# Performance work log

Measured on AMD Instinct MI355X. Metric: run time of the kernel, lower is better.

The kernel has to match this reference:

```python
import jax, jax.numpy as jnp
import numpy as np

N, F_IN, E = 50000, 128, 800000
HID, HEADS, EMB = 32, 8, 64
NEG_SLOPE = 0.2


def gat_conv(x, src, dst, W_src, W_dst, att_src, att_dst, bias, heads, out_ch, concat):
    n = x.shape[0]
    h_src = (x @ W_src).reshape(n, heads, out_ch)   # [N,H,C]
    h_dst = (x @ W_dst).reshape(n, heads, out_ch)
    a_src = jnp.sum(h_src * att_src, axis=-1)       # [N,H]
    a_dst = jnp.sum(h_dst * att_dst, axis=-1)
    e = jax.nn.leaky_relu(a_src[src] + a_dst[dst], NEG_SLOPE)  # [E,H]
    # segment softmax over destination nodes (stable, max detached as in PyG)
    m = jax.ops.segment_max(e, dst, num_segments=n)
    m = jnp.where(jnp.isfinite(m), m, 0.0)
    ex = jnp.exp(e - jax.lax.stop_gradient(m)[dst])
    denom = jax.ops.segment_sum(ex, dst, num_segments=n)
    alpha = ex / (denom[dst] + 1e-16)               # [E,H]
    msg = h_src[src] * alpha[:, :, None]            # [E,H,C]
    out = jax.ops.segment_sum(msg, dst, num_segments=n)  # [N,H,C]
    if concat:
        out = out.reshape(n, heads * out_ch)
    else:
        out = out.mean(axis=1)
    return out + bias


def setup_inputs() -> dict:
    key = jax.random.key(0)
    ks = jax.random.split(key, 12)
    g = lambda k, shape: jax.random.normal(k, shape, dtype=jnp.float32) * (1.0 / np.sqrt(shape[0]))
    x = jax.random.normal(ks[0], (N, F_IN), dtype=jnp.float32)
    edge_index = jax.random.randint(ks[1], (2, E), 0, N, dtype=jnp.int64)
    return {
        "x": x,
        "edge_index": edge_index,
        "W_src1": g(ks[2], (F_IN, HEADS * HID)),
        "W_dst1": g(ks[3], (F_IN, HEADS * HID)),
        "att_src1": g(ks[4], (HEADS, HID)) * 0.1,
        "att_dst1": g(ks[5], (HEADS, HID)) * 0.1,
        "b1": jnp.zeros((HEADS * HID,), dtype=jnp.float32),
        "W_src2": g(ks[6], (HEADS * HID, EMB)),
        "W_dst2": g(ks[7], (HEADS * HID, EMB)),
        "att_src2": g(ks[8], (1, EMB)) * 0.1,
        "att_dst2": g(ks[9], (1, EMB)) * 0.1,
        "b2": jnp.zeros((EMB,), dtype=jnp.float32),
    }


def reference(x, edge_index, W_src1, W_dst1, att_src1, att_dst1, b1,
              W_src2, W_dst2, att_src2, att_dst2, b2):
    src, dst = edge_index[0], edge_index[1]
    h = gat_conv(x, src, dst, W_src1, W_dst1, att_src1, att_dst1, b1, HEADS, HID, True)
    h = jax.nn.relu(h)
    out = gat_conv(h, src, dst, W_src2, W_dst2, att_src2, att_dst2, b2, 1, EMB, False)
    return out
```

## Files before the change

### kernel.cpp

```cpp
#include <hip/hip_runtime.h>
#include <hip/hip_bf16.h>
#include <cstdint>
#include <cstddef>

#define NN    50000
#define FIN   128
#define EE    800000
#define HID_  32
#define HEADS_ 8
#define EMB_  64
#define NEG   0.2f
#define NB_SCAN 196
#define NB_PREP 202
#define NB_EDGE 3125
#define NB_GEMM1 1564
#define LOG2E 1.4426950408889634f

typedef short bf16x8 __attribute__((ext_vector_type(8)));
typedef float f32x4  __attribute__((ext_vector_type(4)));

static __device__ __forceinline__ ushort f2bf(float f){
    uint u = __float_as_uint(f);
    uint r = (u + 0x7FFFu + ((u >> 16) & 1u)) >> 16;
    return (ushort)r;
}
static __device__ __forceinline__ float bf2f(ushort u){
    return __uint_as_float(((uint)u) << 16);
}
static __device__ __forceinline__ float pexp(float t){
    return __builtin_amdgcn_exp2f(fmaxf(t, NEG * t));
}

__global__ __launch_bounds__(256) void k_prep_hist(const float* __restrict__ Wsrc1, const float* __restrict__ Wdst1,
                                                   const float* __restrict__ asrc1, const float* __restrict__ adst1,
                                                   const float* __restrict__ Wsrc2, const float* __restrict__ Wdst2,
                                                   const float* __restrict__ asrc2, const float* __restrict__ adst2,
                                                   ushort* __restrict__ wt1bf, float* __restrict__ wt2,
                                                   ushort* __restrict__ w1t, ushort* __restrict__ w2t,
                                                   const int* __restrict__ dst, int* __restrict__ deg,
                                                   int* __restrict__ rank){
    if (blockIdx.x >= NB_PREP){
        int e = (blockIdx.x - NB_PREP) * 256 + threadIdx.x;
        if (e < EE) rank[e] = atomicAdd(&deg[dst[e]], 1);
        return;
    }
    int idx = blockIdx.x * blockDim.x + threadIdx.x;
    if (idx < 2048){
        int f = idx >> 4, j = idx & 15;
        const float* W; const float* a; int h;
        if (j < 8) { W = Wsrc1; a = asrc1; h = j; } else { W = Wdst1; a = adst1; h = j - 8; }
        float s = 0.f;
        #pragma unroll
        for (int c = 0; c < HID_; ++c)
            s += W[(size_t)f * (HEADS_ * HID_) + h * HID_ + c] * a[h * HID_ + c];
        wt1bf[j * 128 + f] = f2bf(s * LOG2E);
    } else if (idx < 2560){
        int t = idx - 2048;
        int f = t >> 1, j = t & 1;
        const float* W = j ? Wdst2 : Wsrc2;
        const float* a = j ? adst2 : asrc2;
        float s = 0.f;
        #pragma unroll
        for (int c = 0; c < EMB_; ++c) s += W[(size_t)f * EMB_ + c] * a[c];
        wt2[j * 256 + f] = s * LOG2E;
    } else if (idx < 35328){
        int t = idx - 2560;
        int n = t >> 7, k = t & 127;
        w1t[t] = f2bf(Wsrc1[(size_t)k * 256 + n]);
    } else if (idx < 51712){
        int t = idx - 35328;
        int n = t >> 8, k = t & 255;
        w2t[t] = f2bf(Wsrc2[(size_t)k * 64 + n]);
    }
}

__global__ __launch_bounds__(256) void k_scanall(const int* __restrict__ deg, int* __restrict__ row_ptr,
                                                 int* __restrict__ bsum, int* __restrict__ flags){
    __shared__ int s[256];
    __shared__ int ps[256];
    int tid = threadIdx.x, b = blockIdx.x;
    int i = b * 256 + tid;
    int v = (i < NN) ? deg[i] : 0;
    s[tid] = v;
    __syncthreads();
    #pragma unroll
    for (int off = 1; off < 256; off <<= 1){
        int t = (tid >= off) ? s[tid - off] : 0;
        __syncthreads();
        s[tid] += t;
        __syncthreads();
    }
    if (tid == 255){
        bsum[b] = s[255];
        __hip_atomic_store(&flags[b], 1, __ATOMIC_RELEASE, __HIP_MEMORY_SCOPE_AGENT);
    }
    int p = 0;
    if (tid < b){
        while (__hip_atomic_load(&flags[tid], __ATOMIC_ACQUIRE, __HIP_MEMORY_SCOPE_AGENT) == 0){}
        p = bsum[tid];
    }
    ps[tid] = p;
    __syncthreads();
    #pragma unroll
    for (int off = 128; off > 0; off >>= 1){
        if (tid < off) ps[tid] += ps[tid + off];
        __syncthreads();
    }
    int boff = ps[0];
    if (i < NN) row_ptr[i] = boff + s[tid] - v;
    if (b == 0 && tid == 0) row_ptr[NN] = EE;
}

__global__ __launch_bounds__(256) void k_gemm1_scatter(const float* __restrict__ x,
                                                       const ushort* __restrict__ w1t,
                                                       const ushort* __restrict__ wt1bf,
                                                       ushort* __restrict__ c,
                                                       float* __restrict__ a_src1,
                                                       float* __restrict__ a_dst1,
                                                       const int* __restrict__ src, const int* __restrict__ dstp,
                                                       const int* __restrict__ row_ptr, const int* __restrict__ rank,
                                                       int* __restrict__ col){
    __shared__ ushort As[64][136];
    __shared__ ushort Bs[128][136];
    __shared__ ushort Bsa[16][136];
    if (blockIdx.x >= NB_GEMM1){
        int e = (blockIdx.x - NB_GEMM1) * 256 + threadIdx.x;
        if (e < EE){
            int d = dstp[e];
            col[row_ptr[d] + rank[e]] = src[e];
        }
        return;
    }
    const int tid = threadIdx.x;
    const int m0 = (blockIdx.x >> 1) * 64;
    const int n0 = (blockIdx.x & 1) * 128;
    #pragma unroll
    for (int i = 0; i < 8; ++i){
        int idx = tid + i * 256;
        int r = idx >> 5, c4 = idx & 31;
        int m = m0 + r;
        float4 v = make_float4(0.f, 0.f, 0.f, 0.f);
        if (m < NN) v = *(const float4*)&x[(size_t)m * FIN + c4 * 4];
        ushort4 u; u.x = f2bf(v.x); u.y = f2bf(v.y); u.z = f2bf(v.z); u.w = f2bf(v.w);
        *(ushort4*)&As[r][c4 * 4] = u;
    }
    #pragma unroll
    for (int i = 0; i < 8; ++i){
        int idx = tid + i * 256;
        int r = idx >> 4, c8 = idx & 15;
        const ushort4* s4 = (const ushort4*)&w1t[(size_t)(n0 + r) * 128 + c8 * 8];
        *(ushort4*)&Bs[r][c8 * 8]     = s4[0];
        *(ushort4*)&Bs[r][c8 * 8 + 4] = s4[1];
    }
    if (n0 == 0){
        int r = tid >> 4, c8 = tid & 15;
        const ushort4* s4 = (const ushort4*)&wt1bf[r * 128 + c8 * 8];
        *(ushort4*)&Bsa[r][c8 * 8]     = s4[0];
        *(ushort4*)&Bsa[r][c8 * 8 + 4] = s4[1];
    }
    __syncthreads();
    const int lane = tid & 63;
    const int w    = tid >> 6;
    const int mr   = lane & 15;
    const int kg   = lane >> 4;
    f32x4 acc[8];
    #pragma unroll
    for (int i = 0; i < 8; ++i) acc[i] = (f32x4){0.f, 0.f, 0.f, 0.f};
    f32x4 acca = (f32x4){0.f, 0.f, 0.f, 0.f};
    #pragma unroll
    for (int ks = 0; ks < 4; ++ks){
        bf16x8 a = *(const bf16x8*)&As[w * 16 + mr][ks * 32 + kg * 8];
        #pragma unroll
        for (int nf = 0; nf < 8; ++nf){
            bf16x8 b = *(const bf16x8*)&Bs[nf * 16 + mr][ks * 32 + kg * 8];
            acc[nf] = __builtin_amdgcn_mfma_f32_16x16x32_bf16(a, b, acc[nf], 0, 0, 0);
        }
        if (n0 == 0){
            bf16x8 ba = *(const bf16x8*)&Bsa[mr][ks * 32 + kg * 8];
            acca = __builtin_amdgcn_mfma_f32_16x16x32_bf16(a, ba, acca, 0, 0, 0);
        }
    }
    #pragma unroll
    for (int nf = 0; nf < 8; ++nf){
        int colb = n0 + nf * 16 + mr;
        #pragma unroll
        for (int r = 0; r < 4; ++r){
            int row = m0 + w * 16 + kg * 4 + r;
            if (row < NN) c[(size_t)row * 256 + colb] = f2bf(acc[nf][r]);
        }
    }
    if (n0 == 0){
        int j = mr;
        #pragma unroll
        for (int r = 0; r < 4; ++r){
            int row = m0 + w * 16 + kg * 4 + r;
            if (row < NN){
                if (j < 8) a_src1[(size_t)row * 8 + j]       = acca[r];
                else       a_dst1[(size_t)row * 8 + (j - 8)] = acca[r];
            }
        }
    }
}

__global__ __launch_bounds__(256) void k_gemm2_mfma(const ushort* __restrict__ hbf,
                                                    const ushort* __restrict__ w2t,
                                                    ushort* __restrict__ c2){
    __shared__ ushort As[64][264];
    __shared__ ushort Bs[64][264];
    const int tid = threadIdx.x;
    const int m0 = blockIdx.x * 64;
    #pragma unroll
    for (int i = 0; i < 8; ++i){
        int idx = tid + i * 256;
        int r = idx >> 5, c8 = idx & 31;
        int m = m0 + r;
        ushort4 v0 = make_ushort4(0,0,0,0), v1 = make_ushort4(0,0,0,0);
        if (m < NN){
            const ushort4* s4 = (const ushort4*)&hbf[(size_t)m * 256 + c8 * 8];
            v0 = s4[0]; v1 = s4[1];
        }
        *(ushort4*)&As[r][c8 * 8]     = v0;
        *(ushort4*)&As[r][c8 * 8 + 4] = v1;
    }
    #pragma unroll
    for (int i = 0; i < 8; ++i){
        int idx = tid + i * 256;
        int r = idx >> 5, c8 = idx & 31;
        const ushort4* s4 = (const ushort4*)&w2t[(size_t)r * 256 + c8 * 8];
        *(ushort4*)&Bs[r][c8 * 8]     = s4[0];
        *(ushort4*)&Bs[r][c8 * 8 + 4] = s4[1];
    }
    __syncthreads();
    const int lane = tid & 63;
    const int w    = tid >> 6;
    const int mr   = lane & 15;
    const int kg   = lane >> 4;
    f32x4 acc[4];
    #pragma unroll
    for (int i = 0; i < 4; ++i) acc[i] = (f32x4){0.f, 0.f, 0.f, 0.f};
    #pragma unroll
    for (int ks = 0; ks < 8; ++ks){
        bf16x8 a = *(const bf16x8*)&As[w * 16 + mr][ks * 32 + kg * 8];
        #pragma unroll
        for (int nf = 0; nf < 4; ++nf){
            bf16x8 b = *(const bf16x8*)&Bs[nf * 16 + mr][ks * 32 + kg * 8];
            acc[nf] = __builtin_amdgcn_mfma_f32_16x16x32_bf16(a, b, acc[nf], 0, 0, 0);
        }
    }
    #pragma unroll
    for (int nf = 0; nf < 4; ++nf){
        int colb = nf * 16 + mr;
        #pragma unroll
        for (int r = 0; r < 4; ++r){
            int row = m0 + w * 16 + kg * 4 + r;
            if (row < NN) c2[(size_t)row * 64 + colb] = f2bf(acc[nf][r]);
        }
    }
}

__global__ __launch_bounds__(256) void k_agg1(const ushort* __restrict__ hsrc, const float* __restrict__ a_src,
                                              const float* __restrict__ a_dst, const int* __restrict__ row_ptr,
                                              const int* __restrict__ col, const float* __restrict__ b1,
                                              const float* __restrict__ wt2,
                                              ushort* __restrict__ hout_bf,
                                              float* __restrict__ a_src2, float* __restrict__ a_dst2){
    int node = blockIdx.x * 4 + (threadIdx.x >> 6);
    if (node >= NN) return;
    int lane = threadIdx.x & 63;
    int head = lane >> 3;
    float ad = a_dst[(size_t)node * 8 + head];
    const ushort4* h4 = (const ushort4*)hsrc;
    float4 acc = make_float4(0.f, 0.f, 0.f, 0.f);
    float den = 0.f;
    int b = row_ptr[node], en = row_ptr[node + 1];
    int i = b;
    for (; i + 4 <= en; i += 4){
        int s0 = col[i], s1 = col[i+1], s2 = col[i+2], s3 = col[i+3];
        float e0 = a_src[(size_t)s0 * 8 + head];
        float e1 = a_src[(size_t)s1 * 8 + head];
        float e2 = a_src[(size_t)s2 * 8 + head];
        float e3 = a_src[(size_t)s3 * 8 + head];
        ushort4 v0 = h4[(size_t)s0 * 64 + lane];
        ushort4 v1 = h4[(size_t)s1 * 64 + lane];
        ushort4 v2 = h4[(size_t)s2 * 64 + lane];
        ushort4 v3 = h4[(size_t)s3 * 64 + lane];
        float p0 = pexp(e0 + ad);
        float p1 = pexp(e1 + ad);
        float p2 = pexp(e2 + ad);
        float p3 = pexp(e3 + ad);
        acc.x += p0*bf2f(v0.x) + p1*bf2f(v1.x) + p2*bf2f(v2.x) + p3*bf2f(v3.x);
        acc.y += p0*bf2f(v0.y) + p1*bf2f(v1.y) + p2*bf2f(v2.y) + p3*bf2f(v3.y);
        acc.z += p0*bf2f(v0.z) + p1*bf2f(v1.z) + p2*bf2f(v2.z) + p3*bf2f(v3.z);
        acc.w += p0*bf2f(v0.w) + p1*bf2f(v1.w) + p2*bf2f(v2.w) + p3*bf2f(v3.w);
        den += p0 + p1 + p2 + p3;
    }
    for (; i < en; ++i){
        int s = col[i];
        float p = pexp(a_src[(size_t)s * 8 + head] + ad);
        ushort4 v = h4[(size_t)s * 64 + lane];
        acc.x += p * bf2f(v.x); acc.y += p * bf2f(v.y);
        acc.z += p * bf2f(v.z); acc.w += p * bf2f(v.w);
        den += p;
    }
    float inv = 1.f / (den + 1e-16f);
    float4 bb = ((const float4*)b1)[lane];
    float4 o;
    o.x = fmaxf(acc.x * inv + bb.x, 0.f);
    o.y = fmaxf(acc.y * inv + bb.y, 0.f);
    o.z = fmaxf(acc.z * inv + bb.z, 0.f);
    o.w = fmaxf(acc.w * inv + bb.w, 0.f);
    ushort4 ob; ob.x = f2bf(o.x); ob.y = f2bf(o.y); ob.z = f2bf(o.z); ob.w = f2bf(o.w);
    ((ushort4*)hout_bf)[(size_t)node * 64 + lane] = ob;
    float4 ws4 = ((const float4*)wt2)[lane];
    float4 wd4 = ((const float4*)(wt2 + 256))[lane];
    float ss2 = o.x*ws4.x + o.y*ws4.y + o.z*ws4.z + o.w*ws4.w;
    float sd2 = o.x*wd4.x + o.y*wd4.y + o.z*wd4.z + o.w*wd4.w;
    #pragma unroll
    for (int off = 32; off > 0; off >>= 1){
        ss2 += __shfl_xor(ss2, off);
        sd2 += __shfl_xor(sd2, off);
    }
    if (lane == 0){ a_src2[node] = ss2; a_dst2[node] = sd2; }
}

__global__ __launch_bounds__(256) void k_agg2(const ushort* __restrict__ h2bf, const float* __restrict__ a_src2,
                                              const float* __restrict__ a_dst2, const int* __restrict__ row_ptr,
                                              const int* __restrict__ col, const float* __restrict__ b2,
                                              float* __restrict__ out){
    int node = blockIdx.x * 4 + (threadIdx.x >> 6);
    if (node >= NN) return;
    int lane = threadIdx.x & 63;
    float ad = a_dst2[node];
    float acc = 0.f, den = 0.f;
    int b = row_ptr[node], en = row_ptr[node + 1];
    int i = b;
    for (; i + 4 <= en; i += 4){
        int s0 = col[i], s1 = col[i+1], s2 = col[i+2], s3 = col[i+3];
        float e0 = a_src2[s0], e1 = a_src2[s1], e2 = a_src2[s2], e3 = a_src2[s3];
        ushort u0 = h2bf[(size_t)s0 * 64 + lane];
        ushort u1 = h2bf[(size_t)s1 * 64 + lane];
        ushort u2 = h2bf[(size_t)s2 * 64 + lane];
        ushort u3 = h2bf[(size_t)s3 * 64 + lane];
        float p0 = pexp(e0 + ad);
        float p1 = pexp(e1 + ad);
        float p2 = pexp(e2 + ad);
        float p3 = pexp(e3 + ad);
        acc += p0*bf2f(u0) + p1*bf2f(u1) + p2*bf2f(u2) + p3*bf2f(u3);
        den += p0 + p1 + p2 + p3;
    }
    for (; i < en; ++i){
        int s = col[i];
        float p = pexp(a_src2[s] + ad);
        acc += p * bf2f(h2bf[(size_t)s * 64 + lane]);
        den += p;
    }
    out[(size_t)node * 64 + lane] = acc / (den + 1e-16f) + b2[lane];
}

extern "C" void kernel_launch(void* const* d_in, const int* in_sizes, int n_in,
                              void* d_out, int out_size, void* d_ws, size_t ws_size,
                              hipStream_t stream){
    const float* x        = (const float*)d_in[0];
    const int*   ei       = (const int*)  d_in[1];
    const float* Wsrc1    = (const float*)d_in[2];
    const float* Wdst1    = (const float*)d_in[3];
    const float* att_src1 = (const float*)d_in[4];
    const float* att_dst1 = (const float*)d_in[5];
    const float* b1       = (const float*)d_in[6];
    const float* Wsrc2    = (const float*)d_in[7];
    const float* Wdst2    = (const float*)d_in[8];
    const float* att_src2 = (const float*)d_in[9];
    const float* att_dst2 = (const float*)d_in[10];
    const float* b2       = (const float*)d_in[11];
    float* out = (float*)d_out;
    const int* srcp = ei;
    const int* dstp = ei + EE;

    char* base = (char*)d_ws;
    ushort* hbf1   = (ushort*)base;  base += (size_t)NN * 256 * 2;
    ushort* hrel   = (ushort*)base;  base += (size_t)NN * 256 * 2;
    ushort* h2bf   = (ushort*)base;  base += (size_t)NN * 64 * 2;
    float*  a_src1 = (float*)base;   base += (size_t)NN * 8 * 4;
    float*  a_dst1 = (float*)base;   base += (size_t)NN * 8 * 4;
    float*  a_src2 = (float*)base;   base += (size_t)NN * 4;
    float*  a_dst2 = (float*)base;   base += (size_t)NN * 4;
    ushort* wt1bf  = (ushort*)base;  base += 2048 * 2;
    float*  wt2    = (float*)base;   base += 512 * 4;
    ushort* w1t    = (ushort*)base;  base += 32768 * 2;
    ushort* w2t    = (ushort*)base;  base += 16384 * 2;
    int* deg     = (int*)base;       base += (size_t)NN * 4;
    int* flags   = (int*)base;       base += 256 * 4;
    int* row_ptr = (int*)base;       base += (size_t)(NN + 1) * 4;
    int* rank    = (int*)base;       base += (size_t)EE * 4;
    int* col     = (int*)base;       base += (size_t)EE * 4;
    int* bsum    = (int*)base;       base += 256 * 4;

    (void)hipMemsetAsync(deg, 0, (NN + 256) * sizeof(int), stream);

    k_prep_hist<<<NB_PREP + NB_EDGE, 256, 0, stream>>>(Wsrc1, Wdst1, att_src1, att_dst1,
                                                       Wsrc2, Wdst2, att_src2, att_dst2,
                                                       wt1bf, wt2, w1t, w2t,
                                                       dstp, deg, rank);
    k_scanall<<<NB_SCAN, 256, 0, stream>>>(deg, row_ptr, bsum, flags);
    k_gemm1_scatter<<<NB_GEMM1 + NB_EDGE, 256, 0, stream>>>(x, w1t, wt1bf, hbf1, a_src1, a_dst1,
                                                            srcp, dstp, row_ptr, rank, col);
    k_agg1<<<(NN + 3) / 4, 256, 0, stream>>>(hbf1, a_src1, a_dst1, row_ptr, col, b1, wt2,
                                             hrel, a_src2, a_dst2);
    k_gemm2_mfma<<<(NN + 63) / 64, 256, 0, stream>>>(hrel, w2t, h2bf);
    k_agg2<<<(NN + 3) / 4, 256, 0, stream>>>(h2bf, a_src2, a_dst2, row_ptr, col, b2, out);
}
```

Before: 202.7 us.

## Fuse layer-2 GEMM into agg1, overlap GEMM1 half with scan, use cursor scatter

```diff
diff --git a/kernel.cpp b/kernel.cpp
--- a/kernel.cpp
+++ b/kernel.cpp
@@ -13,7 +13,7 @@
 #define NB_SCAN 196
 #define NB_PREP 202
 #define NB_EDGE 3125
-#define NB_GEMM1 1564
+#define NB_M1   782
 #define LOG2E 1.4426950408889634f
 
 typedef short bf16x8 __attribute__((ext_vector_type(8)));
@@ -37,11 +37,10 @@
                                                    const float* __restrict__ asrc2, const float* __restrict__ adst2,
                                                    ushort* __restrict__ wt1bf, float* __restrict__ wt2,
                                                    ushort* __restrict__ w1t, ushort* __restrict__ w2t,
-                                                   const int* __restrict__ dst, int* __restrict__ deg,
-                                                   int* __restrict__ rank){
+                                                   const int* __restrict__ dst, int* __restrict__ deg){
     if (blockIdx.x >= NB_PREP){
         int e = (blockIdx.x - NB_PREP) * 256 + threadIdx.x;
-        if (e < EE) rank[e] = atomicAdd(&deg[dst[e]], 1);
+        if (e < EE) atomicAdd(&deg[dst[e]], 1);
         return;
     }
     int idx = blockIdx.x * blockDim.x + threadIdx.x;
@@ -74,66 +73,51 @@
     }
 }
 
-__global__ __launch_bounds__(256) void k_scanall(const int* __restrict__ deg, int* __restrict__ row_ptr,
-                                                 int* __restrict__ bsum, int* __restrict__ flags){
+__global__ __launch_bounds__(256) void k_scan_gemm1b(const int* __restrict__ deg, int* __restrict__ row_ptr,
+                                                     int* __restrict__ cursor, int* __restrict__ bsum,
+                                                     int* __restrict__ flags,
+                                                     const float* __restrict__ x, const ushort* __restrict__ w1t,
+                                                     ushort* __restrict__ c){
     __shared__ int s[256];
     __shared__ int ps[256];
-    int tid = threadIdx.x, b = blockIdx.x;
-    int i = b * 256 + tid;
-    int v = (i < NN) ? deg[i] : 0;
-    s[tid] = v;
-    __syncthreads();
-    #pragma unroll
-    for (int off = 1; off < 256; off <<= 1){
-        int t = (tid >= off) ? s[tid - off] : 0;
-        __syncthreads();
-        s[tid] += t;
-        __syncthreads();
-    }
-    if (tid == 255){
-        bsum[b] = s[255];
-        __hip_atomic_store(&flags[b], 1, __ATOMIC_RELEASE, __HIP_MEMORY_SCOPE_AGENT);
-    }
-    int p = 0;
-    if (tid < b){
-        while (__hip_atomic_load(&flags[tid], __ATOMIC_ACQUIRE, __HIP_MEMORY_SCOPE_AGENT) == 0){}
-        p = bsum[tid];
-    }
-    ps[tid] = p;
-    __syncthreads();
-    #pragma unroll
-    for (int off = 128; off > 0; off >>= 1){
-        if (tid < off) ps[tid] += ps[tid + off];
-        __syncthreads();
-    }
-    int boff = ps[0];
-    if (i < NN) row_ptr[i] = boff + s[tid] - v;
-    if (b == 0 && tid == 0) row_ptr[NN] = EE;
-}
-
-__global__ __launch_bounds__(256) void k_gemm1_scatter(const float* __restrict__ x,
-                                                       const ushort* __restrict__ w1t,
-                                                       const ushort* __restrict__ wt1bf,
-                                                       ushort* __restrict__ c,
-                                                       float* __restrict__ a_src1,
-                                                       float* __restrict__ a_dst1,
-                                                       const int* __restrict__ src, const int* __restrict__ dstp,
-                                                       const int* __restrict__ row_ptr, const int* __restrict__ rank,
-                                                       int* __restrict__ col){
     __shared__ ushort As[64][136];
     __shared__ ushort Bs[128][136];
-    __shared__ ushort Bsa[16][136];
-    if (blockIdx.x >= NB_GEMM1){
-        int e = (blockIdx.x - NB_GEMM1) * 256 + threadIdx.x;
-        if (e < EE){
-            int d = dstp[e];
-            col[row_ptr[d] + rank[e]] = src[e];
-        }
+    const int tid = threadIdx.x;
+    if (blockIdx.x < NB_SCAN){
+        int b = blockIdx.x;
+        int i = b * 256 + tid;
+        int v = (i < NN) ? deg[i] : 0;
+        s[tid] = v;
+        __syncthreads();
+        #pragma unroll
+        for (int off = 1; off < 256; off <<= 1){
+            int t = (tid >= off) ? s[tid - off] : 0;
+            __syncthreads();
+            s[tid] += t;
+            __syncthreads();
+        }
+        if (tid == 255){
+            bsum[b] = s[255];
+            __hip_atomic_store(&flags[b], 1, __ATOMIC_RELEASE, __HIP_MEMORY_SCOPE_AGENT);
+        }
+        int p = 0;
+        if (tid < b){
+            while (__hip_atomic_load(&flags[tid], __ATOMIC_ACQUIRE, __HIP_MEMORY_SCOPE_AGENT) == 0){}
+            p = bsum[tid];
+        }
+        ps[tid] = p;
+        __syncthreads();
+        #pragma unroll
+        for (int off = 128; off > 0; off >>= 1){
+            if (tid < off) ps[tid] += ps[tid + off];
+            __syncthreads();
+        }
+        int val = ps[0] + s[tid] - v;
+        if (i < NN){ row_ptr[i] = val; cursor[i] = val; }
+        if (b == 0 && tid == 0) row_ptr[NN] = EE;
         return;
     }
-    const int tid = threadIdx.x;
-    const int m0 = (blockIdx.x >> 1) * 64;
-    const int n0 = (blockIdx.x & 1) * 128;
+    const int m0 = (blockIdx.x - NB_SCAN) * 64;
     #pragma unroll
     for (int i = 0; i < 8; ++i){
         int idx = tid + i * 256;
@@ -148,15 +132,9 @@
     for (int i = 0; i < 8; ++i){
         int idx = tid + i * 256;
         int r = idx >> 4, c8 = idx & 15;
-        const ushort4* s4 = (const ushort4*)&w1t[(size_t)(n0 + r) * 128 + c8 * 8];
+        const ushort4* s4 = (const ushort4*)&w1t[(size_t)(128 + r) * 128 + c8 * 8];
         *(ushort4*)&Bs[r][c8 * 8]     = s4[0];
         *(ushort4*)&Bs[r][c8 * 8 + 4] = s4[1];
-    }
-    if (n0 == 0){
-        int r = tid >> 4, c8 = tid & 15;
-        const ushort4* s4 = (const ushort4*)&wt1bf[r * 128 + c8 * 8];
-        *(ushort4*)&Bsa[r][c8 * 8]     = s4[0];
-        *(ushort4*)&Bsa[r][c8 * 8 + 4] = s4[1];
     }
     __syncthreads();
     const int lane = tid & 63;
@@ -166,7 +144,6 @@
     f32x4 acc[8];
     #pragma unroll
     for (int i = 0; i < 8; ++i) acc[i] = (f32x4){0.f, 0.f, 0.f, 0.f};
-    f32x4 acca = (f32x4){0.f, 0.f, 0.f, 0.f};
     #pragma unroll
     for (int ks = 0; ks < 4; ++ks){
         bf16x8 a = *(const bf16x8*)&As[w * 16 + mr][ks * 32 + kg * 8];
@@ -175,21 +152,94 @@
             bf16x8 b = *(const bf16x8*)&Bs[nf * 16 + mr][ks * 32 + kg * 8];
             acc[nf] = __builtin_amdgcn_mfma_f32_16x16x32_bf16(a, b, acc[nf], 0, 0, 0);
         }
-        if (n0 == 0){
-            bf16x8 ba = *(const bf16x8*)&Bsa[mr][ks * 32 + kg * 8];
-            acca = __builtin_amdgcn_mfma_f32_16x16x32_bf16(a, ba, acca, 0, 0, 0);
-        }
     }
     #pragma unroll
     for (int nf = 0; nf < 8; ++nf){
-        int colb = n0 + nf * 16 + mr;
+        int colb = 128 + nf * 16 + mr;
         #pragma unroll
         for (int r = 0; r < 4; ++r){
             int row = m0 + w * 16 + kg * 4 + r;
             if (row < NN) c[(size_t)row * 256 + colb] = f2bf(acc[nf][r]);
         }
     }
-    if (n0 == 0){
+}
+
+__global__ __launch_bounds__(256) void k_gemm1a_scatter(const float* __restrict__ x,
+                                                        const ushort* __restrict__ w1t,
+                                                        const ushort* __restrict__ wt1bf,
+                                                        ushort* __restrict__ c,
+                                                        float* __restrict__ a_src1,
+                                                        float* __restrict__ a_dst1,
+                                                        const int* __restrict__ src, const int* __restrict__ dstp,
+                                                        int* __restrict__ cursor, int* __restrict__ col){
+    __shared__ ushort As[64][136];
+    __shared__ ushort Bs[128][136];
+    __shared__ ushort Bsa[16][136];
+    if (blockIdx.x >= NB_M1){
+        int e = (blockIdx.x - NB_M1) * 256 + threadIdx.x;
+        if (e < EE){
+            int d = dstp[e];
+            int pos = atomicAdd(&cursor[d], 1);
+            col[pos] = src[e];
+        }
+        return;
+    }
+    const int tid = threadIdx.x;
+    const int m0 = blockIdx.x * 64;
+    #pragma unroll
+    for (int i = 0; i < 8; ++i){
+        int idx = tid + i * 256;
+        int r = idx >> 5, c4 = idx & 31;
+        int m = m0 + r;
+        float4 v = make_float4(0.f, 0.f, 0.f, 0.f);
+        if (m < NN) v = *(const float4*)&x[(size_t)m * FIN + c4 * 4];
+        ushort4 u; u.x = f2bf(v.x); u.y = f2bf(v.y); u.z = f2bf(v.z); u.w = f2bf(v.w);
+        *(ushort4*)&As[r][c4 * 4] = u;
+    }
+    #pragma unroll
+    for (int i = 0; i < 8; ++i){
+        int idx = tid + i * 256;
+        int r = idx >> 4, c8 = idx & 15;
+        const ushort4* s4 = (const ushort4*)&w1t[(size_t)r * 128 + c8 * 8];
+        *(ushort4*)&Bs[r][c8 * 8]     = s4[0];
+        *(ushort4*)&Bs[r][c8 * 8 + 4] = s4[1];
+    }
+    {
+        int r = tid >> 4, c8 = tid & 15;
+        const ushort4* s4 = (const ushort4*)&wt1bf[r * 128 + c8 * 8];
+        *(ushort4*)&Bsa[r][c8 * 8]     = s4[0];
+        *(ushort4*)&Bsa[r][c8 * 8 + 4] = s4[1];
+    }
+    __syncthreads();
+    const int lane = tid & 63;
+    const int w    = tid >> 6;
+    const int mr   = lane & 15;
+    const int kg   = lane >> 4;
+    f32x4 acc[8];
+    #pragma unroll
+    for (int i = 0; i < 8; ++i) acc[i] = (f32x4){0.f, 0.f, 0.f, 0.f};
+    f32x4 acca = (f32x4){0.f, 0.f, 0.f, 0.f};
+    #pragma unroll
+    for (int ks = 0; ks < 4; ++ks){
+        bf16x8 a = *(const bf16x8*)&As[w * 16 + mr][ks * 32 + kg * 8];
+        #pragma unroll
+        for (int nf = 0; nf < 8; ++nf){
+            bf16x8 b = *(const bf16x8*)&Bs[nf * 16 + mr][ks * 32 + kg * 8];
+            acc[nf] = __builtin_amdgcn_mfma_f32_16x16x32_bf16(a, b, acc[nf], 0, 0, 0);
+        }
+        bf16x8 ba = *(const bf16x8*)&Bsa[mr][ks * 32 + kg * 8];
+        acca = __builtin_amdgcn_mfma_f32_16x16x32_bf16(a, ba, acca, 0, 0, 0);
+    }
+    #pragma unroll
+    for (int nf = 0; nf < 8; ++nf){
+        int colb = nf * 16 + mr;
+        #pragma unroll
+        for (int r = 0; r < 4; ++r){
+            int row = m0 + w * 16 + kg * 4 + r;
+            if (row < NN) c[(size_t)row * 256 + colb] = f2bf(acc[nf][r]);
+        }
+    }
+    {
         int j = mr;
         #pragma unroll
         for (int r = 0; r < 4; ++r){
@@ -202,72 +252,17 @@
     }
 }
 
-__global__ __launch_bounds__(256) void k_gemm2_mfma(const ushort* __restrict__ hbf,
-                                                    const ushort* __restrict__ w2t,
-                                                    ushort* __restrict__ c2){
-    __shared__ ushort As[64][264];
-    __shared__ ushort Bs[64][264];
-    const int tid = threadIdx.x;
-    const int m0 = blockIdx.x * 64;
-    #pragma unroll
-    for (int i = 0; i < 8; ++i){
-        int idx = tid + i * 256;
-        int r = idx >> 5, c8 = idx & 31;
-        int m = m0 + r;
-        ushort4 v0 = make_ushort4(0,0,0,0), v1 = make_ushort4(0,0,0,0);
-        if (m < NN){
-            const ushort4* s4 = (const ushort4*)&hbf[(size_t)m * 256 + c8 * 8];
-            v0 = s4[0]; v1 = s4[1];
-        }
-        *(ushort4*)&As[r][c8 * 8]     = v0;
-        *(ushort4*)&As[r][c8 * 8 + 4] = v1;
-    }
-    #pragma unroll
-    for (int i = 0; i < 8; ++i){
-        int idx = tid + i * 256;
-        int r = idx >> 5, c8 = idx & 31;
-        const ushort4* s4 = (const ushort4*)&w2t[(size_t)r * 256 + c8 * 8];
-        *(ushort4*)&Bs[r][c8 * 8]     = s4[0];
-        *(ushort4*)&Bs[r][c8 * 8 + 4] = s4[1];
-    }
-    __syncthreads();
-    const int lane = tid & 63;
-    const int w    = tid >> 6;
-    const int mr   = lane & 15;
-    const int kg   = lane >> 4;
-    f32x4 acc[4];
-    #pragma unroll
-    for (int i = 0; i < 4; ++i) acc[i] = (f32x4){0.f, 0.f, 0.f, 0.f};
-    #pragma unroll
-    for (int ks = 0; ks < 8; ++ks){
-        bf16x8 a = *(const bf16x8*)&As[w * 16 + mr][ks * 32 + kg * 8];
-        #pragma unroll
-        for (int nf = 0; nf < 4; ++nf){
-            bf16x8 b = *(const bf16x8*)&Bs[nf * 16 + mr][ks * 32 + kg * 8];
-            acc[nf] = __builtin_amdgcn_mfma_f32_16x16x32_bf16(a, b, acc[nf], 0, 0, 0);
-        }
-    }
-    #pragma unroll
-    for (int nf = 0; nf < 4; ++nf){
-        int colb = nf * 16 + mr;
-        #pragma unroll
-        for (int r = 0; r < 4; ++r){
-            int row = m0 + w * 16 + kg * 4 + r;
-            if (row < NN) c2[(size_t)row * 64 + colb] = f2bf(acc[nf][r]);
-        }
-    }
-}
-
 __global__ __launch_bounds__(256) void k_agg1(const ushort* __restrict__ hsrc, const float* __restrict__ a_src,
                                               const float* __restrict__ a_dst, const int* __restrict__ row_ptr,
                                               const int* __restrict__ col, const float* __restrict__ b1,
-                                              const float* __restrict__ wt2,
-                                              ushort* __restrict__ hout_bf,
+                                              const float* __restrict__ wt2, const ushort* __restrict__ w2t,
+                                              ushort* __restrict__ h2bf,
                                               float* __restrict__ a_src2, float* __restrict__ a_dst2){
-    int node = blockIdx.x * 4 + (threadIdx.x >> 6);
-    if (node >= NN) return;
-    int lane = threadIdx.x & 63;
-    int head = lane >> 3;
+    __shared__ ushort hl[16][264];
+    const int w    = threadIdx.x >> 6;
+    const int node = blockIdx.x * 4 + w;
+    const int lane = threadIdx.x & 63;
+    const int head = lane >> 3;
     float ad = a_dst[(size_t)node * 8 + head];
     const ushort4* h4 = (const ushort4*)hsrc;
     float4 acc = make_float4(0.f, 0.f, 0.f, 0.f);
@@ -309,8 +304,6 @@
     o.y = fmaxf(acc.y * inv + bb.y, 0.f);
     o.z = fmaxf(acc.z * inv + bb.z, 0.f);
     o.w = fmaxf(acc.w * inv + bb.w, 0.f);
-    ushort4 ob; ob.x = f2bf(o.x); ob.y = f2bf(o.y); ob.z = f2bf(o.z); ob.w = f2bf(o.w);
-    ((ushort4*)hout_bf)[(size_t)node * 64 + lane] = ob;
     float4 ws4 = ((const float4*)wt2)[lane];
     float4 wd4 = ((const float4*)(wt2 + 256))[lane];
     float ss2 = o.x*ws4.x + o.y*ws4.y + o.z*ws4.z + o.w*ws4.w;
@@ -321,6 +314,22 @@
         sd2 += __shfl_xor(sd2, off);
     }
     if (lane == 0){ a_src2[node] = ss2; a_dst2[node] = sd2; }
+    ushort4 ob; ob.x = f2bf(o.x); ob.y = f2bf(o.y); ob.z = f2bf(o.z); ob.w = f2bf(o.w);
+    *(ushort4*)&hl[w][lane * 4] = ob;
+    __syncthreads();
+    const int mr = lane & 15, kg = lane >> 4;
+    f32x4 acc2 = (f32x4){0.f, 0.f, 0.f, 0.f};
+    #pragma unroll
+    for (int ks = 0; ks < 8; ++ks){
+        bf16x8 a = *(const bf16x8*)&hl[mr][ks * 32 + kg * 8];
+        bf16x8 bb2 = *(const bf16x8*)&w2t[(size_t)(w * 16 + mr) * 256 + ks * 32 + kg * 8];
+        acc2 = __builtin_amdgcn_mfma_f32_16x16x32_bf16(a, bb2, acc2, 0, 0, 0);
+    }
+    if (kg == 0){
+        #pragma unroll
+        for (int r = 0; r < 4; ++r)
+            h2bf[(size_t)(blockIdx.x * 4 + r) * 64 + w * 16 + mr] = f2bf(acc2[r]);
+    }
 }
 
 __global__ __launch_bounds__(256) void k_agg2(const ushort* __restrict__ h2bf, const float* __restrict__ a_src2,
@@ -334,19 +343,21 @@
     float acc = 0.f, den = 0.f;
     int b = row_ptr[node], en = row_ptr[node + 1];
     int i = b;
-    for (; i + 4 <= en; i += 4){
-        int s0 = col[i], s1 = col[i+1], s2 = col[i+2], s3 = col[i+3];
-        float e0 = a_src2[s0], e1 = a_src2[s1], e2 = a_src2[s2], e3 = a_src2[s3];
-        ushort u0 = h2bf[(size_t)s0 * 64 + lane];
-        ushort u1 = h2bf[(size_t)s1 * 64 + lane];
-        ushort u2 = h2bf[(size_t)s2 * 64 + lane];
-        ushort u3 = h2bf[(size_t)s3 * 64 + lane];
-        float p0 = pexp(e0 + ad);
-        float p1 = pexp(e1 + ad);
-        float p2 = pexp(e2 + ad);
-        float p3 = pexp(e3 + ad);
-        acc += p0*bf2f(u0) + p1*bf2f(u1) + p2*bf2f(u2) + p3*bf2f(u3);
-        den += p0 + p1 + p2 + p3;
+    for (; i + 8 <= en; i += 8){
+        int ss[8]; float e[8]; ushort u[8]; float p[8];
+        #pragma unroll
+        for (int j = 0; j < 8; ++j) ss[j] = col[i + j];
+        #pragma unroll
+        for (int j = 0; j < 8; ++j) e[j] = a_src2[ss[j]];
+        #pragma unroll
+        for (int j = 0; j < 8; ++j) u[j] = h2bf[(size_t)ss[j] * 64 + lane];
+        #pragma unroll
+        for (int j = 0; j < 8; ++j) p[j] = pexp(e[j] + ad);
+        #pragma unroll
+        for (int j = 0; j < 8; ++j){
+            acc += p[j] * bf2f(u[j]);
+            den += p[j];
+        }
     }
     for (; i < en; ++i){
         int s = col[i];
@@ -378,7 +389,6 @@
 
     char* base = (char*)d_ws;
     ushort* hbf1   = (ushort*)base;  base += (size_t)NN * 256 * 2;
-    ushort* hrel   = (ushort*)base;  base += (size_t)NN * 256 * 2;
     ushort* h2bf   = (ushort*)base;  base += (size_t)NN * 64 * 2;
     float*  a_src1 = (float*)base;   base += (size_t)NN * 8 * 4;
     float*  a_dst1 = (float*)base;   base += (size_t)NN * 8 * 4;
@@ -391,7 +401,7 @@
     int* deg     = (int*)base;       base += (size_t)NN * 4;
     int* flags   = (int*)base;       base += 256 * 4;
     int* row_ptr = (int*)base;       base += (size_t)(NN + 1) * 4;
-    int* rank    = (int*)base;       base += (size_t)EE * 4;
+    int* cursor  = (int*)base;       base += (size_t)NN * 4;
     int* col     = (int*)base;       base += (size_t)EE * 4;
     int* bsum    = (int*)base;       base += 256 * 4;
 
@@ -400,12 +410,12 @@
     k_prep_hist<<<NB_PREP + NB_EDGE, 256, 0, stream>>>(Wsrc1, Wdst1, att_src1, att_dst1,
                                                        Wsrc2, Wdst2, att_src2, att_dst2,
                                                        wt1bf, wt2, w1t, w2t,
-                                                       dstp, deg, rank);
-    k_scanall<<<NB_SCAN, 256, 0, stream>>>(deg, row_ptr, bsum, flags);
-    k_gemm1_scatter<<<NB_GEMM1 + NB_EDGE, 256, 0, stream>>>(x, w1t, wt1bf, hbf1, a_src1, a_dst1,
-                                                            srcp, dstp, row_ptr, rank, col);
-    k_agg1<<<(NN + 3) / 4, 256, 0, stream>>>(hbf1, a_src1, a_dst1, row_ptr, col, b1, wt2,
-                                             hrel, a_src2, a_dst2);
-    k_gemm2_mfma<<<(NN + 63) / 64, 256, 0, stream>>>(hrel, w2t, h2bf);
-    k_agg2<<<(NN + 3) / 4, 256, 0, stream>>>(h2bf, a_src2, a_dst2, row_ptr, col, b2, out);
-}
+                                                       dstp, deg);
+    k_scan_gemm1b<<<NB_SCAN + NB_M1, 256, 0, stream>>>(deg, row_ptr, cursor, bsum, flags,
+                                                       x, w1t, hbf1);
+    k_gemm1a_scatter<<<NB_M1 + NB_EDGE, 256, 0, stream>>>(x, w1t, wt1bf, hbf1, a_src1, a_dst1,
+                                                          srcp, dstp, cursor, col);
+    k_agg1<<<NN / 4, 256, 0, stream>>>(hbf1, a_src1, a_dst1, row_ptr, col, b1, wt2, w2t,
+                                       h2bf, a_src2, a_dst2);
+    k_agg2<<<NN / 4, 256, 0, stream>>>(h2bf, a_src2, a_dst2, row_ptr, col, b2, out);
+}
```

New measurement: 265.9 us. 31.2% more time.

## Replace CSR scan and scatter with fixed-capacity per-node edge buckets

Applied to the files above, without the earlier changes.

```diff
diff --git a/kernel.cpp b/kernel.cpp
--- a/kernel.cpp
+++ b/kernel.cpp
@@ -10,10 +10,9 @@
 #define HEADS_ 8
 #define EMB_  64
 #define NEG   0.2f
-#define NB_SCAN 196
+#define CAP   64
 #define NB_PREP 202
 #define NB_EDGE 3125
-#define NB_GEMM1 1564
 #define LOG2E 1.4426950408889634f
 
 typedef short bf16x8 __attribute__((ext_vector_type(8)));
@@ -37,11 +36,15 @@
                                                    const float* __restrict__ asrc2, const float* __restrict__ adst2,
                                                    ushort* __restrict__ wt1bf, float* __restrict__ wt2,
                                                    ushort* __restrict__ w1t, ushort* __restrict__ w2t,
-                                                   const int* __restrict__ dst, int* __restrict__ deg,
-                                                   int* __restrict__ rank){
+                                                   const int* __restrict__ src, const int* __restrict__ dst,
+                                                   int* __restrict__ deg, int* __restrict__ col){
     if (blockIdx.x >= NB_PREP){
         int e = (blockIdx.x - NB_PREP) * 256 + threadIdx.x;
-        if (e < EE) rank[e] = atomicAdd(&deg[dst[e]], 1);
+        if (e < EE){
+            int d = dst[e];
+            int r = atomicAdd(&deg[d], 1);
+            col[d * CAP + r] = src[e];
+        }
         return;
     }
     int idx = blockIdx.x * blockDim.x + threadIdx.x;
@@ -74,66 +77,18 @@
     }
 }
 
-__global__ __launch_bounds__(256) void k_scanall(const int* __restrict__ deg, int* __restrict__ row_ptr,
-                                                 int* __restrict__ bsum, int* __restrict__ flags){
-    __shared__ int s[256];
-    __shared__ int ps[256];
-    int tid = threadIdx.x, b = blockIdx.x;
-    int i = b * 256 + tid;
-    int v = (i < NN) ? deg[i] : 0;
-    s[tid] = v;
-    __syncthreads();
-    #pragma unroll
-    for (int off = 1; off < 256; off <<= 1){
-        int t = (tid >= off) ? s[tid - off] : 0;
-        __syncthreads();
-        s[tid] += t;
-        __syncthreads();
-    }
-    if (tid == 255){
-        bsum[b] = s[255];
-        __hip_atomic_store(&flags[b], 1, __ATOMIC_RELEASE, __HIP_MEMORY_SCOPE_AGENT);
-    }
-    int p = 0;
-    if (tid < b){
-        while (__hip_atomic_load(&flags[tid], __ATOMIC_ACQUIRE, __HIP_MEMORY_SCOPE_AGENT) == 0){}
-        p = bsum[tid];
-    }
-    ps[tid] = p;
-    __syncthreads();
-    #pragma unroll
-    for (int off = 128; off > 0; off >>= 1){
-        if (tid < off) ps[tid] += ps[tid + off];
-        __syncthreads();
-    }
-    int boff = ps[0];
-    if (i < NN) row_ptr[i] = boff + s[tid] - v;
-    if (b == 0 && tid == 0) row_ptr[NN] = EE;
-}
-
-__global__ __launch_bounds__(256) void k_gemm1_scatter(const float* __restrict__ x,
-                                                       const ushort* __restrict__ w1t,
-                                                       const ushort* __restrict__ wt1bf,
-                                                       ushort* __restrict__ c,
-                                                       float* __restrict__ a_src1,
-                                                       float* __restrict__ a_dst1,
-                                                       const int* __restrict__ src, const int* __restrict__ dstp,
-                                                       const int* __restrict__ row_ptr, const int* __restrict__ rank,
-                                                       int* __restrict__ col){
+__global__ __launch_bounds__(256) void k_gemm1_mfma(const float* __restrict__ x,
+                                                    const ushort* __restrict__ w1t,
+                                                    const ushort* __restrict__ wt1bf,
+                                                    ushort* __restrict__ c,
+                                                    float* __restrict__ a_src1,
+                                                    float* __restrict__ a_dst1){
     __shared__ ushort As[64][136];
     __shared__ ushort Bs[128][136];
     __shared__ ushort Bsa[16][136];
-    if (blockIdx.x >= NB_GEMM1){
-        int e = (blockIdx.x - NB_GEMM1) * 256 + threadIdx.x;
-        if (e < EE){
-            int d = dstp[e];
-            col[row_ptr[d] + rank[e]] = src[e];
-        }
-        return;
-    }
     const int tid = threadIdx.x;
-    const int m0 = (blockIdx.x >> 1) * 64;
-    const int n0 = (blockIdx.x & 1) * 128;
+    const int m0 = blockIdx.x * 64;
+    const int n0 = blockIdx.y * 128;
     #pragma unroll
     for (int i = 0; i < 8; ++i){
         int idx = tid + i * 256;
@@ -152,7 +107,7 @@
         *(ushort4*)&Bs[r][c8 * 8]     = s4[0];
         *(ushort4*)&Bs[r][c8 * 8 + 4] = s4[1];
     }
-    if (n0 == 0){
+    if (blockIdx.y == 0){
         int r = tid >> 4, c8 = tid & 15;
         const ushort4* s4 = (const ushort4*)&wt1bf[r * 128 + c8 * 8];
         *(ushort4*)&Bsa[r][c8 * 8]     = s4[0];
@@ -175,7 +130,7 @@
             bf16x8 b = *(const bf16x8*)&Bs[nf * 16 + mr][ks * 32 + kg * 8];
             acc[nf] = __builtin_amdgcn_mfma_f32_16x16x32_bf16(a, b, acc[nf], 0, 0, 0);
         }
-        if (n0 == 0){
+        if (blockIdx.y == 0){
             bf16x8 ba = *(const bf16x8*)&Bsa[mr][ks * 32 + kg * 8];
             acca = __builtin_amdgcn_mfma_f32_16x16x32_bf16(a, ba, acca, 0, 0, 0);
         }
@@ -189,7 +144,7 @@
             if (row < NN) c[(size_t)row * 256 + colb] = f2bf(acc[nf][r]);
         }
     }
-    if (n0 == 0){
+    if (blockIdx.y == 0){
         int j = mr;
         #pragma unroll
         for (int r = 0; r < 4; ++r){
@@ -202,64 +157,8 @@
     }
 }
 
-__global__ __launch_bounds__(256) void k_gemm2_mfma(const ushort* __restrict__ hbf,
-                                                    const ushort* __restrict__ w2t,
-                                                    ushort* __restrict__ c2){
-    __shared__ ushort As[64][264];
-    __shared__ ushort Bs[64][264];
-    const int tid = threadIdx.x;
-    const int m0 = blockIdx.x * 64;
-    #pragma unroll
-    for (int i = 0; i < 8; ++i){
-        int idx = tid + i * 256;
-        int r = idx >> 5, c8 = idx & 31;
-        int m = m0 + r;
-        ushort4 v0 = make_ushort4(0,0,0,0), v1 = make_ushort4(0,0,0,0);
-        if (m < NN){
-            const ushort4* s4 = (const ushort4*)&hbf[(size_t)m * 256 + c8 * 8];
-            v0 = s4[0]; v1 = s4[1];
-        }
-        *(ushort4*)&As[r][c8 * 8]     = v0;
-        *(ushort4*)&As[r][c8 * 8 + 4] = v1;
-    }
-    #pragma unroll
-    for (int i = 0; i < 8; ++i){
-        int idx = tid + i * 256;
-        int r = idx >> 5, c8 = idx & 31;
-        const ushort4* s4 = (const ushort4*)&w2t[(size_t)r * 256 + c8 * 8];
-        *(ushort4*)&Bs[r][c8 * 8]     = s4[0];
-        *(ushort4*)&Bs[r][c8 * 8 + 4] = s4[1];
-    }
-    __syncthreads();
-    const int lane = tid & 63;
-    const int w    = tid >> 6;
-    const int mr   = lane & 15;
-    const int kg   = lane >> 4;
-    f32x4 acc[4];
-    #pragma unroll
-    for (int i = 0; i < 4; ++i) acc[i] = (f32x4){0.f, 0.f, 0.f, 0.f};
-    #pragma unroll
-    for (int ks = 0; ks < 8; ++ks){
-        bf16x8 a = *(const bf16x8*)&As[w * 16 + mr][ks * 32 + kg * 8];
-        #pragma unroll
-        for (int nf = 0; nf < 4; ++nf){
-            bf16x8 b = *(const bf16x8*)&Bs[nf * 16 + mr][ks * 32 + kg * 8];
-            acc[nf] = __builtin_amdgcn_mfma_f32_16x16x32_bf16(a, b, acc[nf], 0, 0, 0);
-        }
-    }
-    #pragma unroll
-    for (int nf = 0; nf < 4; ++nf){
-        int colb = nf * 16 + mr;
-        #pragma unroll
-        for (int r = 0; r < 4; ++r){
-            int row = m0 + w * 16 + kg * 4 + r;
-            if (row < NN) c2[(size_t)row * 64 + colb] = f2bf(acc[nf][r]);
-        }
-    }
-}
-
 __global__ __launch_bounds__(256) void k_agg1(const ushort* __restrict__ hsrc, const float* __restrict__ a_src,
-                                              const float* __restrict__ a_dst, const int* __restrict__ row_ptr,
+                                              const float* __restrict__ a_dst, const int* __restrict__ deg,
                                               const int* __restrict__ col, const float* __restrict__ b1,
                                               const float* __restrict__ wt2,
                                               ushort* __restrict__ hout_bf,
@@ -272,7 +171,7 @@
     const ushort4* h4 = (const ushort4*)hsrc;
     float4 acc = make_float4(0.f, 0.f, 0.f, 0.f);
     float den = 0.f;
-    int b = row_ptr[node], en = row_ptr[node + 1];
+    int b = node * CAP, en = b + deg[node];
     int i = b;
     for (; i + 4 <= en; i += 4){
         int s0 = col[i], s1 = col[i+1], s2 = col[i+2], s3 = col[i+3];
@@ -323,8 +222,64 @@
     if (lane == 0){ a_src2[node] = ss2; a_dst2[node] = sd2; }
 }
 
+__global__ __launch_bounds__(256) void k_gemm2_mfma(const ushort* __restrict__ hbf,
+                                                    const ushort* __restrict__ w2t,
+                                                    ushort* __restrict__ c2){
+    __shared__ ushort As[64][264];
+    __shared__ ushort Bs[64][264];
+    const int tid = threadIdx.x;
+    const int m0 = blockIdx.x * 64;
+    #pragma unroll
+    for (int i = 0; i < 8; ++i){
+        int idx = tid + i * 256;
+        int r = idx >> 5, c8 = idx & 31;
+        int m = m0 + r;
+        ushort4 v0 = make_ushort4(0,0,0,0), v1 = make_ushort4(0,0,0,0);
+        if (m < NN){
+            const ushort4* s4 = (const ushort4*)&hbf[(size_t)m * 256 + c8 * 8];
+            v0 = s4[0]; v1 = s4[1];
+        }
+        *(ushort4*)&As[r][c8 * 8]     = v0;
+        *(ushort4*)&As[r][c8 * 8 + 4] = v1;
+    }
+    #pragma unroll
+    for (int i = 0; i < 8; ++i){
+        int idx = tid + i * 256;
+        int r = idx >> 5, c8 = idx & 31;
+        const ushort4* s4 = (const ushort4*)&w2t[(size_t)r * 256 + c8 * 8];
+        *(ushort4*)&Bs[r][c8 * 8]     = s4[0];
+        *(ushort4*)&Bs[r][c8 * 8 + 4] = s4[1];
+    }
+    __syncthreads();
+    const int lane = tid & 63;
+    const int w    = tid >> 6;
+    const int mr   = lane & 15;
+    const int kg   = lane >> 4;
+    f32x4 acc[4];
+    #pragma unroll
+    for (int i = 0; i < 4; ++i) acc[i] = (f32x4){0.f, 0.f, 0.f, 0.f};
+    #pragma unroll
+    for (int ks = 0; ks < 8; ++ks){
+        bf16x8 a = *(const bf16x8*)&As[w * 16 + mr][ks * 32 + kg * 8];
+        #pragma unroll
+        for (int nf = 0; nf < 4; ++nf){
+            bf16x8 b = *(const bf16x8*)&Bs[nf * 16 + mr][ks * 32 + kg * 8];
+            acc[nf] = __builtin_amdgcn_mfma_f32_16x16x32_bf16(a, b, acc[nf], 0, 0, 0);
+        }
+    }
+    #pragma unroll
+    for (int nf = 0; nf < 4; ++nf){
+        int colb = nf * 16 + mr;
+        #pragma unroll
+        for (int r = 0; r < 4; ++r){
+            int row = m0 + w * 16 + kg * 4 + r;
+            if (row < NN) c2[(size_t)row * 64 + colb] = f2bf(acc[nf][r]);
+        }
+    }
+}
+
 __global__ __launch_bounds__(256) void k_agg2(const ushort* __restrict__ h2bf, const float* __restrict__ a_src2,
-                                              const float* __restrict__ a_dst2, const int* __restrict__ row_ptr,
+                                              const float* __restrict__ a_dst2, const int* __restrict__ deg,
                                               const int* __restrict__ col, const float* __restrict__ b2,
                                               float* __restrict__ out){
     int node = blockIdx.x * 4 + (threadIdx.x >> 6);
@@ -332,21 +287,23 @@
     int lane = threadIdx.x & 63;
     float ad = a_dst2[node];
     float acc = 0.f, den = 0.f;
-    int b = row_ptr[node], en = row_ptr[node + 1];
+    int b = node * CAP, en = b + deg[node];
     int i = b;
-    for (; i + 4 <= en; i += 4){
-        int s0 = col[i], s1 = col[i+1], s2 = col[i+2], s3 = col[i+3];
-        float e0 = a_src2[s0], e1 = a_src2[s1], e2 = a_src2[s2], e3 = a_src2[s3];
-        ushort u0 = h2bf[(size_t)s0 * 64 + lane];
-        ushort u1 = h2bf[(size_t)s1 * 64 + lane];
-        ushort u2 = h2bf[(size_t)s2 * 64 + lane];
-        ushort u3 = h2bf[(size_t)s3 * 64 + lane];
-        float p0 = pexp(e0 + ad);
-        float p1 = pexp(e1 + ad);
-        float p2 = pexp(e2 + ad);
-        float p3 = pexp(e3 + ad);
-        acc += p0*bf2f(u0) + p1*bf2f(u1) + p2*bf2f(u2) + p3*bf2f(u3);
-        den += p0 + p1 + p2 + p3;
+    for (; i + 8 <= en; i += 8){
+        int ss[8]; float e[8]; ushort u[8]; float p[8];
+        #pragma unroll
+        for (int j = 0; j < 8; ++j) ss[j] = col[i + j];
+        #pragma unroll
+        for (int j = 0; j < 8; ++j) e[j] = a_src2[ss[j]];
+        #pragma unroll
+        for (int j = 0; j < 8; ++j) u[j] = h2bf[(size_t)ss[j] * 64 + lane];
+        #pragma unroll
+        for (int j = 0; j < 8; ++j) p[j] = pexp(e[j] + ad);
+        #pragma unroll
+        for (int j = 0; j < 8; ++j){
+            acc += p[j] * bf2f(u[j]);
+            den += p[j];
+        }
     }
     for (; i < en; ++i){
         int s = col[i];
@@ -389,23 +346,18 @@
     ushort* w1t    = (ushort*)base;  base += 32768 * 2;
     ushort* w2t    = (ushort*)base;  base += 16384 * 2;
     int* deg     = (int*)base;       base += (size_t)NN * 4;
-    int* flags   = (int*)base;       base += 256 * 4;
-    int* row_ptr = (int*)base;       base += (size_t)(NN + 1) * 4;
-    int* rank    = (int*)base;       base += (size_t)EE * 4;
-    int* col     = (int*)base;       base += (size_t)EE * 4;
-    int* bsum    = (int*)base;       base += 256 * 4;
-
-    (void)hipMemsetAsync(deg, 0, (NN + 256) * sizeof(int), stream);
+    int* col     = (int*)base;       base += (size_t)NN * CAP * 4;
+
+    (void)hipMemsetAsync(deg, 0, NN * sizeof(int), stream);
 
     k_prep_hist<<<NB_PREP + NB_EDGE, 256, 0, stream>>>(Wsrc1, Wdst1, att_src1, att_dst1,
                                                        Wsrc2, Wdst2, att_src2, att_dst2,
                                                        wt1bf, wt2, w1t, w2t,
-                                                       dstp, deg, rank);
-    k_scanall<<<NB_SCAN, 256, 0, stream>>>(deg, row_ptr, bsum, flags);
-    k_gemm1_scatter<<<NB_GEMM1 + NB_EDGE, 256, 0, stream>>>(x, w1t, wt1bf, hbf1, a_src1, a_dst1,
-                                                            srcp, dstp, row_ptr, rank, col);
-    k_agg1<<<(NN + 3) / 4, 256, 0, stream>>>(hbf1, a_src1, a_dst1, row_ptr, col, b1, wt2,
+                                                       srcp, dstp, deg, col);
+    dim3 g1((NN + 63) / 64, 2);
+    k_gemm1_mfma<<<g1, 256, 0, stream>>>(x, w1t, wt1bf, hbf1, a_src1, a_dst1);
+    k_agg1<<<(NN + 3) / 4, 256, 0, stream>>>(hbf1, a_src1, a_dst1, deg, col, b1, wt2,
                                              hrel, a_src2, a_dst2);
     k_gemm2_mfma<<<(NN + 63) / 64, 256, 0, stream>>>(hrel, w2t, h2bf);
-    k_agg2<<<(NN + 3) / 4, 256, 0, stream>>>(h2bf, a_src2, a_dst2, row_ptr, col, b2, out);
-}
+    k_agg2<<<(NN + 3) / 4, 256, 0, stream>>>(h2bf, a_src2, a_dst2, deg, col, b2, out);
+}
```

Result: slower. 208.4 us (+2.8%).
